# Performance work log

Hardware: AMD Instinct MI355X
Metric: run time of the kernel (lower is better)

## Reference

```python
import jax, jax.numpy as jnp
import numpy as np

LSTM_IN = 125
LSTM_H = 125
MLP_D_H = 512
N = 512


def _lstm_scan(x, Wih, Whh, bih, bhh):
    # x: (N, LSTM_IN); PyTorch gate order: i, f, g, o
    H = LSTM_H
    def step(carry, xt):
        h, c = carry
        g = Wih @ xt + Whh @ h + bih + bhh  # (4H,)
        i = jax.nn.sigmoid(g[:H])
        f = jax.nn.sigmoid(g[H:2 * H])
        gg = jnp.tanh(g[2 * H:3 * H])
        o = jax.nn.sigmoid(g[3 * H:])
        c = f * c + i * gg
        h = o * jnp.tanh(c)
        return (h, c), h
    init = (jnp.zeros((H,), x.dtype), jnp.zeros((H,), x.dtype))
    _, hs = jax.lax.scan(step, init, x)
    return hs  # (N, H)


def setup_inputs() -> dict:
    key = jax.random.key(0)
    ks = jax.random.split(key, 14)
    s = 0.05
    d = {
        "sentence_emb": jax.random.normal(ks[0], (N, 1, LSTM_IN), jnp.float32),
        "Wih_f": jax.random.normal(ks[1], (4 * LSTM_H, LSTM_IN), jnp.float32) * s,
        "Whh_f": jax.random.normal(ks[2], (4 * LSTM_H, LSTM_H), jnp.float32) * s,
        "bih_f": jax.random.normal(ks[3], (4 * LSTM_H,), jnp.float32) * s,
        "bhh_f": jax.random.normal(ks[4], (4 * LSTM_H,), jnp.float32) * s,
        "Wih_b": jax.random.normal(ks[5], (4 * LSTM_H, LSTM_IN), jnp.float32) * s,
        "Whh_b": jax.random.normal(ks[6], (4 * LSTM_H, LSTM_H), jnp.float32) * s,
        "bih_b": jax.random.normal(ks[7], (4 * LSTM_H,), jnp.float32) * s,
        "bhh_b": jax.random.normal(ks[8], (4 * LSTM_H,), jnp.float32) * s,
        "W1": jax.random.normal(ks[9], (MLP_D_H, 4 * LSTM_H), jnp.float32) * s,
        "b1": jax.random.normal(ks[10], (MLP_D_H,), jnp.float32) * s,
        "W2": jax.random.normal(ks[11], (1, MLP_D_H), jnp.float32) * s,
        "b2": jax.random.normal(ks[12], (1,), jnp.float32) * s,
    }
    return d


def reference(sentence_emb, Wih_f, Whh_f, bih_f, bhh_f, Wih_b, Whh_b, bih_b, bhh_b, W1, b1, W2, b2):
    x = sentence_emb[:, 0, :]  # (N, 125), batch=1
    h_fwd = _lstm_scan(x, Wih_f, Whh_f, bih_f, bhh_f)           # (N, 125)
    h_bwd = _lstm_scan(x[::-1], Wih_b, Whh_b, bih_b, bhh_b)[::-1]  # (N, 125)
    h = jnp.concatenate([h_fwd, h_bwd], axis=-1)  # (N, 250)
    # output_mtx[i, j] = MLP(concat(h[j], h[i]))
    # Decompose first linear: W1 @ cat(h_j, h_i) = Wa @ h_j + Wb @ h_i
    D = h.shape[-1]
    Pa = h @ W1[:, :D].T   # (N, H): contribution of h_j
    Pb = h @ W1[:, D:].T   # (N, H): contribution of h_i
    hidden = jnp.tanh(Pb[:, None, :] + Pa[None, :, :] + b1)  # (N, N, H)
    out = hidden @ W2[0] + b2[0]  # (N, N)
    return out
```

## Files before the change

### kernel.cpp

```cpp
#include <hip/hip_runtime.h>

typedef __bf16 bf16_t;
typedef __bf16 bf16x8 __attribute__((ext_vector_type(8)));
typedef float f32x4 __attribute__((ext_vector_type(4)));
typedef int   int4v __attribute__((ext_vector_type(4)));

#define LOG2E 1.4426950408889634f

template<int CTRL>
__device__ __forceinline__ float qperm(float x) {
  return __builtin_bit_cast(float,
      __builtin_amdgcn_update_dpp(0, __builtin_bit_cast(int, x), CTRL, 0xF, 0xF, true));
}

__device__ __forceinline__ void lds_barrier() {
  asm volatile("s_waitcnt lgkmcnt(0)\n\ts_barrier" ::: "memory");
}

__global__ __launch_bounds__(256) void pre_kernel(
    const float* __restrict__ x,
    const float* __restrict__ Wih_f, const float* __restrict__ bih_f,
    const float* __restrict__ bhh_f,
    const float* __restrict__ Wih_b, const float* __restrict__ bih_b,
    const float* __restrict__ bhh_b,
    float* __restrict__ preT)
{
  const int dir = blockIdx.x >> 5;
  const int T   = blockIdx.x & 31;
  const float* __restrict__ Wih = dir ? Wih_b : Wih_f;
  const float* __restrict__ bih = dir ? bih_b : bih_f;
  const float* __restrict__ bhh = dir ? bhh_b : bhh_f;

  const int tid = threadIdx.x;
  const int wv  = tid >> 6;
  const int lane = tid & 63;
  const int q = lane >> 4, cc = lane & 15;

  const int r  = 16 * T + cc;
  const int na = r >> 2, pa = r & 3;
  const bool vld = (na < 125);
  const float* __restrict__ Wr = Wih + (vld ? (125 * pa + na) * 125 : 0);

  bf16x8 whi[4], wlo[4];
  #pragma unroll
  for (int ks = 0; ks < 4; ++ks) {
    #pragma unroll
    for (int j = 0; j < 8; ++j) {
      int k = 32 * ks + 8 * q + j;
      float wvv = (vld && k < 125) ? Wr[k] : 0.0f;
      bf16_t hi = (bf16_t)wvv;
      whi[ks][j] = hi;
      wlo[ks][j] = (bf16_t)(wvv - (float)hi);
    }
  }

  float bias[4];
  #pragma unroll
  for (int reg = 0; reg < 4; ++reg) {
    int ro = 16 * T + 4 * q + reg;
    int no = ro >> 2, po = ro & 3;
    bias[reg] = (no < 125) ? (bih[125 * po + no] + bhh[125 * po + no]) : 0.0f;
  }

  for (int i = 0; i < 8; ++i) {
    const int tt = 8 * wv + i;
    const int t  = 16 * tt + cc;
    const int trow = dir ? (511 - t) : t;
    const float* __restrict__ xr = x + trow * 125;

    f32x4 acc = (f32x4)0.0f;
    #pragma unroll
    for (int ks = 0; ks < 4; ++ks) {
      bf16x8 xhi, xlo;
      #pragma unroll
      for (int j = 0; j < 8; ++j) {
        int k = 32 * ks + 8 * q + j;
        float xv = (k < 125) ? xr[k] : 0.0f;
        bf16_t hi = (bf16_t)xv;
        xhi[j] = hi;
        xlo[j] = (bf16_t)(xv - (float)hi);
      }
      acc = __builtin_amdgcn_mfma_f32_16x16x32_bf16(whi[ks], xhi, acc, 0, 0, 0);
      acc = __builtin_amdgcn_mfma_f32_16x16x32_bf16(whi[ks], xlo, acc, 0, 0, 0);
      acc = __builtin_amdgcn_mfma_f32_16x16x32_bf16(wlo[ks], xhi, acc, 0, 0, 0);
    }
    #pragma unroll
    for (int reg = 0; reg < 4; ++reg) {
      int ro = 16 * T + 4 * q + reg;
      preT[dir * 262144 + ro * 512 + 16 * tt + cc] = acc[reg] + bias[reg];
    }
  }
}

__global__ __launch_bounds__(512) void lstm_kernel(
    const float* __restrict__ Whh_f, const float* __restrict__ Whh_b,
    const float* __restrict__ pre,
    bf16_t* __restrict__ h_all)
{
  const int dir = blockIdx.x;
  const float* __restrict__ Whh = dir ? Whh_b : Whh_f;

  const int tid  = threadIdx.x;
  const int lane = tid & 63;
  const int w    = tid >> 6;
  const int q    = lane >> 4;
  const int cc   = lane & 15;
  const int lt   = cc >> 2;
  const int p    = cc & 3;

  float wm = 0.0f;
  #pragma unroll
  for (int LT = 0; LT < 4; ++LT) {
    int rr = 16 * (4 * w + LT) + cc;
    int nn = rr >> 2, pp = rr & 3;
    if (nn < 125) {
      const float* __restrict__ Wrow = Whh + (125 * pp + nn) * 125;
      #pragma unroll
      for (int ks = 0; ks < 2; ++ks)
        #pragma unroll
        for (int jj = 0; jj < 16; ++jj) {
          int k = 64 * ks + 16 * q + jj;
          if (k < 125) wm = fmaxf(wm, fabsf(Wrow[k]));
        }
    }
  }
  #pragma unroll
  for (int off = 1; off < 64; off <<= 1)
    wm = fmaxf(wm, __shfl_xor(wm, off));
  __shared__ float wmx[8];
  if (lane == 0) wmx[w] = wm;
  __syncthreads();
  float wmax = wmx[0];
  #pragma unroll
  for (int u = 1; u < 8; ++u) wmax = fmaxf(wmax, wmx[u]);
  const float s_w  = 127.0f / wmax;
  const float invq = wmax / (127.0f * 127.0f);

  int4v afrag[4][2];
  #pragma unroll
  for (int LT = 0; LT < 4; ++LT) {
    int rr = 16 * (4 * w + LT) + cc;
    int nn = rr >> 2, pp = rr & 3;
    bool avld = (nn < 125);
    const float* __restrict__ Wrow = Whh + (avld ? (125 * pp + nn) * 125 : 0);
    #pragma unroll
    for (int ks = 0; ks < 2; ++ks) {
      int4v v;
      #pragma unroll
      for (int word = 0; word < 4; ++word) {
        int b = 0;
        #pragma unroll
        for (int byte = 0; byte < 4; ++byte) {
          int jj = 4 * word + byte;
          int k  = 64 * ks + 16 * q + jj;
          int qv = 0;
          if (avld && k < 125)
            qv = (int)__builtin_rintf(Wrow[k] * s_w);
          b |= (qv & 0xFF) << (8 * byte);
        }
        v[word] = b;
      }
      afrag[LT][ks] = v;
    }
  }

  __shared__ __align__(16) char hbuf[2][128];
  if (tid < 256) hbuf[tid >> 7][tid & 127] = 0;
  if (dir == 0) {
    #pragma unroll
    for (int u = 0; u < 6; ++u) h_all[tid * 256 + 250 + u] = (bf16_t)0.0f;
  }
  __syncthreads();

  const int   r_lane = 64 * w + 16 * lt + 4 * q + p;
  const int   nset   = 16 * w + 4 * lt + q;
  const float mult   = (p == 2) ? (-2.0f * LOG2E) : (-LOG2E);
  const float sA     = (p == 2) ? 2.0f : 1.0f;
  const float sB     = (p == 2) ? -1.0f : 0.0f;
  const float dscale = mult * invq;
  const float* __restrict__ preR = pre + dir * 262144 + r_lane * 512;
  float c = 0.0f;

  float4 pv_cur = *(const float4*)preR;

  for (int g = 0; g < 128; ++g) {
    float4 pv_nxt = make_float4(0.f, 0.f, 0.f, 0.f);
    if (g < 127) pv_nxt = *(const float4*)(preR + 4 * (g + 1));

    #pragma unroll
    for (int s4 = 0; s4 < 4; ++s4) {
      const int step = 4 * g + s4;
      const int cur  = s4 & 1, nxt = cur ^ 1;
      const float pv = (s4 == 0) ? pv_cur.x : (s4 == 1) ? pv_cur.y
                     : (s4 == 2) ? pv_cur.z : pv_cur.w;
      const float pvm = mult * pv;

      int4v b0 = *(const int4v*)&hbuf[cur][16 * q];
      int4v b1 = *(const int4v*)&hbuf[cur][64 + 16 * q];

      int4v acc[4];
      #pragma unroll
      for (int LT = 0; LT < 4; ++LT) {
        int4v a = (int4v)0;
        a = __builtin_amdgcn_mfma_i32_16x16x64_i8(afrag[LT][0], b0, a, 0, 0, 0);
        a = __builtin_amdgcn_mfma_i32_16x16x64_i8(afrag[LT][1], b1, a, 0, 0, 0);
        acc[LT] = a;
      }

      int gl[4];
      #pragma unroll
      for (int LT = 0; LT < 4; ++LT) {
        int a01 = (p & 1) ? acc[LT][1] : acc[LT][0];
        int a23 = (p & 1) ? acc[LT][3] : acc[LT][2];
        gl[LT] = (p & 2) ? a23 : a01;
      }
      int b01 = (lt & 1) ? gl[1] : gl[0];
      int b23 = (lt & 1) ? gl[3] : gl[2];
      int gsel = (lt & 2) ? b23 : b01;

      float gf  = (float)gsel;
      float xg  = fmaf(gf, dscale, pvm);
      float e   = __builtin_amdgcn_exp2f(xg);
      float y   = __builtin_amdgcn_rcpf(1.0f + e);
      float act = fmaf(y, sA, sB);

      float b_i = qperm<0x00>(act);
      float b_f = qperm<0x55>(act);
      float b_g = qperm<0xAA>(act);
      float b_o = qperm<0xFF>(act);
      c = fmaf(b_f, c, b_i * b_g);
      float e2 = __builtin_amdgcn_exp2f(-2.0f * LOG2E * c);
      float tc = fmaf(__builtin_amdgcn_rcpf(1.0f + e2), 2.0f, -1.0f);
      float h  = b_o * tc;

      if (p == 0) {
        int qh = (int)__builtin_rintf(h * 127.0f);
        hbuf[nxt][nset] = (char)qh;
        if (nset < 125) {
          int t_orig = dir ? (511 - step) : step;
          h_all[t_orig * 256 + dir * 125 + nset] = (bf16_t)h;
        }
      }
      lds_barrier();
    }
    pv_cur = pv_nxt;
  }
}

__global__ __launch_bounds__(256) void qgemm_kernel(
    const bf16_t* __restrict__ h_all,
    const float* __restrict__ W1,
    const float* __restrict__ b1,
    float* __restrict__ Ea,
    float* __restrict__ Eb)
{
  const int tid  = threadIdx.x;
  const int wv   = tid >> 6;
  const int lane = tid & 63;
  const int q    = lane >> 4, cc = lane & 15;
  const int bj   = blockIdx.x & 31;
  const int bm   = blockIdx.x >> 5;
  const int m    = bm * 64 + wv * 16 + cc;
  const int j0   = bj * 16;
  const int jA   = j0 + cc;

  const bool isB = (m >= 512);
  const int  row = isB ? (m - 512) : m;
  const int  cof = isB ? 250 : 0;

  f32x4 acc = (f32x4)0.0f;
  #pragma unroll
  for (int ks = 0; ks < 8; ++ks) {
    int kb = 32 * ks + 8 * q;
    bf16x8 a = *(const bf16x8*)&h_all[jA * 256 + kb];
    bf16x8 b;
    #pragma unroll
    for (int jj = 0; jj < 8; ++jj) {
      int k = kb + jj;
      float v = (k < 250) ? W1[row * 500 + cof + k] : 0.0f;
      b[jj] = (bf16_t)v;
    }
    acc = __builtin_amdgcn_mfma_f32_16x16x32_bf16(a, b, acc, 0, 0, 0);
  }

  const float C2 = 2.0f * LOG2E;
  #pragma unroll
  for (int reg = 0; reg < 4; ++reg) {
    int j = j0 + 4 * q + reg;
    float v = acc[reg];
    if (!isB) Ea[j * 512 + m] = __builtin_amdgcn_exp2f(C2 * v);
    else      Eb[j * 512 + (m - 512)] =
                  __builtin_amdgcn_exp2f(C2 * (v + b1[m - 512]));
  }
}

__global__ __launch_bounds__(256) void outer_kernel(
    const float* __restrict__ Ea, const float* __restrict__ Eb,
    const float* __restrict__ W2, const float* __restrict__ b2,
    float* __restrict__ out)
{
  __shared__ float sa2[2][32][36];
  __shared__ float sb2[2][16][36];
  __shared__ float sw[2][32];

  const int tid = threadIdx.x;
  const int bi  = blockIdx.x >> 4;
  const int bjx = blockIdx.x & 15;
  const int i0  = bi * 16, j0 = bjx * 32;
  const int ii  = tid & 15;
  const int jj2 = tid >> 4;

  const int lj  = tid & 31, lk4 = (tid >> 5) * 4;
  const int li  = tid & 15, lk4b = ((tid >> 4) & 7) * 4;

  float accR0 = 0.0f, accR1 = 0.0f;
  float wsum = 0.0f;

  for (int kc = 0; kc < 16; ++kc) {
    const int buf = kc & 1;
    const int k0  = kc * 32;
    float4 va = *(const float4*)&Ea[(j0 + lj) * 512 + k0 + lk4];
    *(float4*)&sa2[buf][lj][lk4] = va;
    if (tid < 128) {
      float4 vb = *(const float4*)&Eb[(i0 + li) * 512 + k0 + lk4b];
      *(float4*)&sb2[buf][li][lk4b] = vb;
    }
    if (tid < 32) sw[buf][tid] = W2[k0 + tid];
    __syncthreads();

    #pragma unroll 4
    for (int kk = 0; kk < 32; kk += 2) {
      float2 wv = *(const float2*)&sw[buf][kk];
      float2 bv = *(const float2*)&sb2[buf][ii][kk];
      float2 a0 = *(const float2*)&sa2[buf][2 * jj2 + 0][kk];
      float2 a1 = *(const float2*)&sa2[buf][2 * jj2 + 1][kk];
      wsum += wv.x + wv.y;
      {
        float t1  = fmaf(a0.x, bv.x, 1.0f);
        float t2  = fmaf(a0.y, bv.y, 1.0f);
        float den = t1 * t2;
        float num = fmaf(wv.x, t2, wv.y * t1);
        accR0 = fmaf(num, __builtin_amdgcn_rcpf(den), accR0);
      }
      {
        float t1  = fmaf(a1.x, bv.x, 1.0f);
        float t2  = fmaf(a1.y, bv.y, 1.0f);
        float den = t1 * t2;
        float num = fmaf(wv.x, t2, wv.y * t1);
        accR1 = fmaf(num, __builtin_amdgcn_rcpf(den), accR1);
      }
    }
  }

  const float bb = b2[0];
  float2 o;
  o.x = wsum - 2.0f * accR0 + bb;
  o.y = wsum - 2.0f * accR1 + bb;
  *(float2*)&out[(i0 + ii) * 512 + j0 + 2 * jj2] = o;
}

extern "C" void kernel_launch(void* const* d_in, const int* in_sizes, int n_in,
                              void* d_out, int out_size, void* d_ws, size_t ws_size,
                              hipStream_t stream) {
  const float* emb   = (const float*)d_in[0];
  const float* Wih_f = (const float*)d_in[1];
  const float* Whh_f = (const float*)d_in[2];
  const float* bih_f = (const float*)d_in[3];
  const float* bhh_f = (const float*)d_in[4];
  const float* Wih_b = (const float*)d_in[5];
  const float* Whh_b = (const float*)d_in[6];
  const float* bih_b = (const float*)d_in[7];
  const float* bhh_b = (const float*)d_in[8];
  const float* W1    = (const float*)d_in[9];
  const float* b1    = (const float*)d_in[10];
  const float* W2    = (const float*)d_in[11];
  const float* b2    = (const float*)d_in[12];
  float* out = (float*)d_out;

  char* ws = (char*)d_ws;
  float*  pre   = (float*)ws;
  bf16_t* h_all = (bf16_t*)(ws + 2 * 1024 * 1024);
  float*  Ea    = (float*)(ws + 2 * 1024 * 1024 + 256 * 1024);
  float*  Eb    = Ea + 512 * 512;

  pre_kernel<<<64, 256, 0, stream>>>(emb, Wih_f, bih_f, bhh_f,
                                     Wih_b, bih_b, bhh_b, pre);
  lstm_kernel<<<2, 512, 0, stream>>>(Whh_f, Whh_b, pre, h_all);
  qgemm_kernel<<<512, 256, 0, stream>>>(h_all, W1, b1, Ea, Eb);
  outer_kernel<<<512, 256, 0, stream>>>(Ea, Eb, W2, b2, out);
}
```

Before: 318.9 us.

## Fuse all four stages into one persistent kernel with atomic grid barriers

Merges the input-projection, LSTM recurrence, W1 GEMM and outer MLP kernels into a single 256-block launch separated by software grid barriers built on an atomic counter. The aim is to remove the launch gaps and tail effects between four small kernels, which matter most around the latency-bound LSTM stage. Costs: a memset is added before the launch, the LSTM phase still runs on only two blocks while the rest spin on the barrier, and correctness depends on all 256 blocks of 512 threads being co-resident.

```diff
diff --git a/kernel.cpp b/kernel.cpp
--- a/kernel.cpp
+++ b/kernel.cpp
@@ -6,6 +6,7 @@
 typedef int   int4v __attribute__((ext_vector_type(4)));
 
 #define LOG2E 1.4426950408889634f
+#define NBLK  256
 
 template<int CTRL>
 __device__ __forceinline__ float qperm(float x) {
@@ -17,53 +18,75 @@
   asm volatile("s_waitcnt lgkmcnt(0)\n\ts_barrier" ::: "memory");
 }
 
-__global__ __launch_bounds__(256) void pre_kernel(
+__device__ __forceinline__ void gridbar(unsigned* cnt, unsigned target) {
+  __syncthreads();
+  if (threadIdx.x == 0) {
+    __threadfence();
+    __hip_atomic_fetch_add(cnt, 1u, __ATOMIC_RELEASE, __HIP_MEMORY_SCOPE_AGENT);
+    while (__hip_atomic_load(cnt, __ATOMIC_ACQUIRE, __HIP_MEMORY_SCOPE_AGENT)
+           < target)
+      __builtin_amdgcn_s_sleep(16);
+  }
+  __syncthreads();
+}
+
+__global__ __launch_bounds__(512) void fused_kernel(
     const float* __restrict__ x,
     const float* __restrict__ Wih_f, const float* __restrict__ bih_f,
     const float* __restrict__ bhh_f,
     const float* __restrict__ Wih_b, const float* __restrict__ bih_b,
     const float* __restrict__ bhh_b,
-    float* __restrict__ preT)
+    const float* __restrict__ Whh_f, const float* __restrict__ Whh_b,
+    const float* __restrict__ W1,    const float* __restrict__ b1,
+    const float* __restrict__ W2,    const float* __restrict__ b2,
+    float* __restrict__ preT,
+    bf16_t* __restrict__ h_all,
+    float* __restrict__ Ea,
+    float* __restrict__ Eb,
+    unsigned* __restrict__ cnt,
+    float* __restrict__ out)
 {
-  const int dir = blockIdx.x >> 5;
-  const int T   = blockIdx.x & 31;
-  const float* __restrict__ Wih = dir ? Wih_b : Wih_f;
-  const float* __restrict__ bih = dir ? bih_b : bih_f;
-  const float* __restrict__ bhh = dir ? bhh_b : bhh_f;
-
-  const int tid = threadIdx.x;
-  const int wv  = tid >> 6;
+  const int tid  = threadIdx.x;
+  const int wv   = tid >> 6;
   const int lane = tid & 63;
-  const int q = lane >> 4, cc = lane & 15;
-
-  const int r  = 16 * T + cc;
-  const int na = r >> 2, pa = r & 3;
-  const bool vld = (na < 125);
-  const float* __restrict__ Wr = Wih + (vld ? (125 * pa + na) * 125 : 0);
-
-  bf16x8 whi[4], wlo[4];
-  #pragma unroll
-  for (int ks = 0; ks < 4; ++ks) {
-    #pragma unroll
-    for (int j = 0; j < 8; ++j) {
-      int k = 32 * ks + 8 * q + j;
-      float wvv = (vld && k < 125) ? Wr[k] : 0.0f;
-      bf16_t hi = (bf16_t)wvv;
-      whi[ks][j] = hi;
-      wlo[ks][j] = (bf16_t)(wvv - (float)hi);
-    }
-  }
-
-  float bias[4];
-  #pragma unroll
-  for (int reg = 0; reg < 4; ++reg) {
-    int ro = 16 * T + 4 * q + reg;
-    int no = ro >> 2, po = ro & 3;
-    bias[reg] = (no < 125) ? (bih[125 * po + no] + bhh[125 * po + no]) : 0.0f;
-  }
-
-  for (int i = 0; i < 8; ++i) {
-    const int tt = 8 * wv + i;
+  const int q    = lane >> 4, cc = lane & 15;
+
+  {
+    const int b   = blockIdx.x;
+    const int dir = b >> 7;
+    const int T   = (b >> 2) & 31;
+    const int tq  = b & 3;
+    const float* __restrict__ Wih = dir ? Wih_b : Wih_f;
+    const float* __restrict__ bih = dir ? bih_b : bih_f;
+    const float* __restrict__ bhh = dir ? bhh_b : bhh_f;
+
+    const int r  = 16 * T + cc;
+    const int na = r >> 2, pa = r & 3;
+    const bool vld = (na < 125);
+    const float* __restrict__ Wr = Wih + (vld ? (125 * pa + na) * 125 : 0);
+
+    bf16x8 whi[4], wlo[4];
+    #pragma unroll
+    for (int ks = 0; ks < 4; ++ks) {
+      #pragma unroll
+      for (int j = 0; j < 8; ++j) {
+        int k = 32 * ks + 8 * q + j;
+        float wvv = (vld && k < 125) ? Wr[k] : 0.0f;
+        bf16_t hi = (bf16_t)wvv;
+        whi[ks][j] = hi;
+        wlo[ks][j] = (bf16_t)(wvv - (float)hi);
+      }
+    }
+
+    float bias[4];
+    #pragma unroll
+    for (int reg = 0; reg < 4; ++reg) {
+      int ro = 16 * T + 4 * q + reg;
+      int no = ro >> 2, po = ro & 3;
+      bias[reg] = (no < 125) ? (bih[125 * po + no] + bhh[125 * po + no]) : 0.0f;
+    }
+
+    const int tt = 8 * tq + wv;
     const int t  = 16 * tt + cc;
     const int trow = dir ? (511 - t) : t;
     const float* __restrict__ xr = x + trow * 125;
@@ -90,273 +113,260 @@
       preT[dir * 262144 + ro * 512 + 16 * tt + cc] = acc[reg] + bias[reg];
     }
   }
-}
-
-__global__ __launch_bounds__(512) void lstm_kernel(
-    const float* __restrict__ Whh_f, const float* __restrict__ Whh_b,
-    const float* __restrict__ pre,
-    bf16_t* __restrict__ h_all)
-{
-  const int dir = blockIdx.x;
-  const float* __restrict__ Whh = dir ? Whh_b : Whh_f;
-
-  const int tid  = threadIdx.x;
-  const int lane = tid & 63;
-  const int w    = tid >> 6;
-  const int q    = lane >> 4;
-  const int cc   = lane & 15;
-  const int lt   = cc >> 2;
-  const int p    = cc & 3;
-
-  float wm = 0.0f;
-  #pragma unroll
-  for (int LT = 0; LT < 4; ++LT) {
-    int rr = 16 * (4 * w + LT) + cc;
-    int nn = rr >> 2, pp = rr & 3;
-    if (nn < 125) {
-      const float* __restrict__ Wrow = Whh + (125 * pp + nn) * 125;
-      #pragma unroll
-      for (int ks = 0; ks < 2; ++ks)
+
+  gridbar(cnt, NBLK);
+
+  __shared__ float wmx[8];
+  __shared__ __align__(16) char hbuf[2][128];
+
+  if (blockIdx.x < 2) {
+    const int dir = blockIdx.x;
+    const float* __restrict__ Whh = dir ? Whh_b : Whh_f;
+
+    const int w  = wv;
+    const int lt = cc >> 2;
+    const int p  = cc & 3;
+
+    float wm = 0.0f;
+    #pragma unroll
+    for (int LT = 0; LT < 4; ++LT) {
+      int rr = 16 * (4 * w + LT) + cc;
+      int nn = rr >> 2, pp = rr & 3;
+      if (nn < 125) {
+        const float* __restrict__ Wrow = Whh + (125 * pp + nn) * 125;
         #pragma unroll
-        for (int jj = 0; jj < 16; ++jj) {
-          int k = 64 * ks + 16 * q + jj;
-          if (k < 125) wm = fmaxf(wm, fabsf(Wrow[k]));
-        }
+        for (int ks = 0; ks < 2; ++ks)
+          #pragma unroll
+          for (int jj = 0; jj < 16; ++jj) {
+            int k = 64 * ks + 16 * q + jj;
+            if (k < 125) wm = fmaxf(wm, fabsf(Wrow[k]));
+          }
+      }
+    }
+    #pragma unroll
+    for (int off = 1; off < 64; off <<= 1)
+      wm = fmaxf(wm, __shfl_xor(wm, off));
+    if (lane == 0) wmx[w] = wm;
+    __syncthreads();
+    float wmax = wmx[0];
+    #pragma unroll
+    for (int u = 1; u < 8; ++u) wmax = fmaxf(wmax, wmx[u]);
+    const float s_w  = 127.0f / wmax;
+    const float invq = wmax / (127.0f * 127.0f);
+
+    int4v afrag[4][2];
+    #pragma unroll
+    for (int LT = 0; LT < 4; ++LT) {
+      int rr = 16 * (4 * w + LT) + cc;
+      int nn = rr >> 2, pp = rr & 3;
+      bool avld = (nn < 125);
+      const float* __restrict__ Wrow = Whh + (avld ? (125 * pp + nn) * 125 : 0);
+      #pragma unroll
+      for (int ks = 0; ks < 2; ++ks) {
+        int4v v;
+        #pragma unroll
+        for (int word = 0; word < 4; ++word) {
+          int bb = 0;
+          #pragma unroll
+          for (int byte = 0; byte < 4; ++byte) {
+            int jj = 4 * word + byte;
+            int k  = 64 * ks + 16 * q + jj;
+            int qv = 0;
+            if (avld && k < 125)
+              qv = (int)__builtin_rintf(Wrow[k] * s_w);
+            bb |= (qv & 0xFF) << (8 * byte);
+          }
+          v[word] = bb;
+        }
+        afrag[LT][ks] = v;
+      }
+    }
+
+    if (tid < 256) hbuf[tid >> 7][tid & 127] = 0;
+    if (dir == 0) {
+      #pragma unroll
+      for (int u = 0; u < 6; ++u) h_all[tid * 256 + 250 + u] = (bf16_t)0.0f;
+    }
+    __syncthreads();
+
+    const int   r_lane = 64 * w + 16 * lt + 4 * q + p;
+    const int   nset   = 16 * w + 4 * lt + q;
+    const float mult   = (p == 2) ? (-2.0f * LOG2E) : (-LOG2E);
+    const float sA     = (p == 2) ? 2.0f : 1.0f;
+    const float sB     = (p == 2) ? -1.0f : 0.0f;
+    const float dscale = mult * invq;
+    const float* __restrict__ preR = preT + dir * 262144 + r_lane * 512;
+    float c = 0.0f;
+
+    float4 pv_cur = *(const float4*)preR;
+
+    for (int g = 0; g < 128; ++g) {
+      float4 pv_nxt = make_float4(0.f, 0.f, 0.f, 0.f);
+      if (g < 127) pv_nxt = *(const float4*)(preR + 4 * (g + 1));
+
+      #pragma unroll
+      for (int s4 = 0; s4 < 4; ++s4) {
+        const int step = 4 * g + s4;
+        const int cur  = s4 & 1, nxt = cur ^ 1;
+        const float pv = (s4 == 0) ? pv_cur.x : (s4 == 1) ? pv_cur.y
+                       : (s4 == 2) ? pv_cur.z : pv_cur.w;
+        const float pvm = mult * pv;
+
+        int4v b0 = *(const int4v*)&hbuf[cur][16 * q];
+        int4v b1 = *(const int4v*)&hbuf[cur][64 + 16 * q];
+
+        int4v acc[4];
+        #pragma unroll
+        for (int LT = 0; LT < 4; ++LT) {
+          int4v a = (int4v)0;
+          a = __builtin_amdgcn_mfma_i32_16x16x64_i8(afrag[LT][0], b0, a, 0, 0, 0);
+          a = __builtin_amdgcn_mfma_i32_16x16x64_i8(afrag[LT][1], b1, a, 0, 0, 0);
+          acc[LT] = a;
+        }
+
+        int gl[4];
+        #pragma unroll
+        for (int LT = 0; LT < 4; ++LT) {
+          int a01 = (p & 1) ? acc[LT][1] : acc[LT][0];
+          int a23 = (p & 1) ? acc[LT][3] : acc[LT][2];
+          gl[LT] = (p & 2) ? a23 : a01;
+        }
+        int b01 = (lt & 1) ? gl[1] : gl[0];
+        int b23 = (lt & 1) ? gl[3] : gl[2];
+        int gsel = (lt & 2) ? b23 : b01;
+
+        float gf  = (float)gsel;
+        float xg  = fmaf(gf, dscale, pvm);
+        float e   = __builtin_amdgcn_exp2f(xg);
+        float y   = __builtin_amdgcn_rcpf(1.0f + e);
+        float act = fmaf(y, sA, sB);
+
+        float b_i = qperm<0x00>(act);
+        float b_f = qperm<0x55>(act);
+        float b_g = qperm<0xAA>(act);
+        float b_o = qperm<0xFF>(act);
+        c = fmaf(b_f, c, b_i * b_g);
+        float e2 = __builtin_amdgcn_exp2f(-2.0f * LOG2E * c);
+        float tc = fmaf(__builtin_amdgcn_rcpf(1.0f + e2), 2.0f, -1.0f);
+        float h  = b_o * tc;
+
+        if (p == 0) {
+          int qh = (int)__builtin_rintf(h * 127.0f);
+          hbuf[nxt][nset] = (char)qh;
+          if (nset < 125) {
+            int t_orig = dir ? (511 - step) : step;
+            h_all[t_orig * 256 + dir * 125 + nset] = (bf16_t)h;
+          }
+        }
+        lds_barrier();
+      }
+      pv_cur = pv_nxt;
     }
   }
-  #pragma unroll
-  for (int off = 1; off < 64; off <<= 1)
-    wm = fmaxf(wm, __shfl_xor(wm, off));
-  __shared__ float wmx[8];
-  if (lane == 0) wmx[w] = wm;
-  __syncthreads();
-  float wmax = wmx[0];
-  #pragma unroll
-  for (int u = 1; u < 8; ++u) wmax = fmaxf(wmax, wmx[u]);
-  const float s_w  = 127.0f / wmax;
-  const float invq = wmax / (127.0f * 127.0f);
-
-  int4v afrag[4][2];
-  #pragma unroll
-  for (int LT = 0; LT < 4; ++LT) {
-    int rr = 16 * (4 * w + LT) + cc;
-    int nn = rr >> 2, pp = rr & 3;
-    bool avld = (nn < 125);
-    const float* __restrict__ Wrow = Whh + (avld ? (125 * pp + nn) * 125 : 0);
-    #pragma unroll
-    for (int ks = 0; ks < 2; ++ks) {
-      int4v v;
-      #pragma unroll
-      for (int word = 0; word < 4; ++word) {
-        int b = 0;
-        #pragma unroll
-        for (int byte = 0; byte < 4; ++byte) {
-          int jj = 4 * word + byte;
-          int k  = 64 * ks + 16 * q + jj;
-          int qv = 0;
-          if (avld && k < 125)
-            qv = (int)__builtin_rintf(Wrow[k] * s_w);
-          b |= (qv & 0xFF) << (8 * byte);
-        }
-        v[word] = b;
-      }
-      afrag[LT][ks] = v;
+
+  gridbar(cnt, 2 * NBLK);
+
+  {
+    const int job = blockIdx.x * 8 + wv;
+    const int bj  = job & 31;
+    const int mg  = job >> 5;
+    const int m   = mg * 16 + cc;
+    const int j0  = bj * 16;
+    const int jA  = j0 + cc;
+
+    const bool isB = (m >= 512);
+    const int  row = isB ? (m - 512) : m;
+    const int  cof = isB ? 250 : 0;
+
+    f32x4 acc = (f32x4)0.0f;
+    #pragma unroll
+    for (int ks = 0; ks < 8; ++ks) {
+      int kb = 32 * ks + 8 * q;
+      bf16x8 a = *(const bf16x8*)&h_all[jA * 256 + kb];
+      bf16x8 bfr;
+      #pragma unroll
+      for (int jj = 0; jj < 8; ++jj) {
+        int k = kb + jj;
+        float v = (k < 250) ? W1[row * 500 + cof + k] : 0.0f;
+        bfr[jj] = (bf16_t)v;
+      }
+      acc = __builtin_amdgcn_mfma_f32_16x16x32_bf16(a, bfr, acc, 0, 0, 0);
+    }
+
+    const float C2 = 2.0f * LOG2E;
+    #pragma unroll
+    for (int reg = 0; reg < 4; ++reg) {
+      int j = j0 + 4 * q + reg;
+      float v = acc[reg];
+      if (!isB) Ea[j * 512 + m] = __builtin_amdgcn_exp2f(C2 * v);
+      else      Eb[j * 512 + (m - 512)] =
+                    __builtin_amdgcn_exp2f(C2 * (v + b1[m - 512]));
     }
   }
 
-  __shared__ __align__(16) char hbuf[2][128];
-  if (tid < 256) hbuf[tid >> 7][tid & 127] = 0;
-  if (dir == 0) {
-    #pragma unroll
-    for (int u = 0; u < 6; ++u) h_all[tid * 256 + 250 + u] = (bf16_t)0.0f;
+  gridbar(cnt, 3 * NBLK);
+
+  {
+    __shared__ float sa2[2][2][32][36];
+    __shared__ float sb2[2][2][16][36];
+    __shared__ float sw[2][2][32];
+
+    const int half = tid >> 8;
+    const int t2   = tid & 255;
+    const int job  = blockIdx.x * 2 + half;
+    const int bi   = job >> 4, bjx = job & 15;
+    const int i0   = bi * 16, j0 = bjx * 32;
+    const int ii   = t2 & 15;
+    const int jj2  = t2 >> 4;
+
+    const int lj  = t2 & 31, lk4 = (t2 >> 5) * 4;
+    const int li  = t2 & 15, lk4b = ((t2 >> 4) & 7) * 4;
+
+    float accR0 = 0.0f, accR1 = 0.0f;
+    float wsum = 0.0f;
+
+    for (int kc = 0; kc < 16; ++kc) {
+      const int buf = kc & 1;
+      const int k0  = kc * 32;
+      float4 va = *(const float4*)&Ea[(j0 + lj) * 512 + k0 + lk4];
+      *(float4*)&sa2[half][buf][lj][lk4] = va;
+      if (t2 < 128) {
+        float4 vb = *(const float4*)&Eb[(i0 + li) * 512 + k0 + lk4b];
+        *(float4*)&sb2[half][buf][li][lk4b] = vb;
+      }
+      if (t2 < 32) sw[half][buf][t2] = W2[k0 + t2];
+      __syncthreads();
+
+      #pragma unroll 4
+      for (int kk = 0; kk < 32; kk += 2) {
+        float2 wv2 = *(const float2*)&sw[half][buf][kk];
+        float2 bv  = *(const float2*)&sb2[half][buf][ii][kk];
+        float2 a0  = *(const float2*)&sa2[half][buf][2 * jj2 + 0][kk];
+        float2 a1  = *(const float2*)&sa2[half][buf][2 * jj2 + 1][kk];
+        wsum += wv2.x + wv2.y;
+        {
+          float t1  = fmaf(a0.x, bv.x, 1.0f);
+          float tt2 = fmaf(a0.y, bv.y, 1.0f);
+          float den = t1 * tt2;
+          float num = fmaf(wv2.x, tt2, wv2.y * t1);
+          accR0 = fmaf(num, __builtin_amdgcn_rcpf(den), accR0);
+        }
+        {
+          float t1  = fmaf(a1.x, bv.x, 1.0f);
+          float tt2 = fmaf(a1.y, bv.y, 1.0f);
+          float den = t1 * tt2;
+          float num = fmaf(wv2.x, tt2, wv2.y * t1);
+          accR1 = fmaf(num, __builtin_amdgcn_rcpf(den), accR1);
+        }
+      }
+    }
+
+    const float bb = b2[0];
+    float2 o;
+    o.x = wsum - 2.0f * accR0 + bb;
+    o.y = wsum - 2.0f * accR1 + bb;
+    *(float2*)&out[(i0 + ii) * 512 + j0 + 2 * jj2] = o;
   }
-  __syncthreads();
-
-  const int   r_lane = 64 * w + 16 * lt + 4 * q + p;
-  const int   nset   = 16 * w + 4 * lt + q;
-  const float mult   = (p == 2) ? (-2.0f * LOG2E) : (-LOG2E);
-  const float sA     = (p == 2) ? 2.0f : 1.0f;
-  const float sB     = (p == 2) ? -1.0f : 0.0f;
-  const float dscale = mult * invq;
-  const float* __restrict__ preR = pre + dir * 262144 + r_lane * 512;
-  float c = 0.0f;
-
-  float4 pv_cur = *(const float4*)preR;
-
-  for (int g = 0; g < 128; ++g) {
-    float4 pv_nxt = make_float4(0.f, 0.f, 0.f, 0.f);
-    if (g < 127) pv_nxt = *(const float4*)(preR + 4 * (g + 1));
-
-    #pragma unroll
-    for (int s4 = 0; s4 < 4; ++s4) {
-      const int step = 4 * g + s4;
-      const int cur  = s4 & 1, nxt = cur ^ 1;
-      const float pv = (s4 == 0) ? pv_cur.x : (s4 == 1) ? pv_cur.y
-                     : (s4 == 2) ? pv_cur.z : pv_cur.w;
-      const float pvm = mult * pv;
-
-      int4v b0 = *(const int4v*)&hbuf[cur][16 * q];
-      int4v b1 = *(const int4v*)&hbuf[cur][64 + 16 * q];
-
-      int4v acc[4];
-      #pragma unroll
-      for (int LT = 0; LT < 4; ++LT) {
-        int4v a = (int4v)0;
-        a = __builtin_amdgcn_mfma_i32_16x16x64_i8(afrag[LT][0], b0, a, 0, 0, 0);
-        a = __builtin_amdgcn_mfma_i32_16x16x64_i8(afrag[LT][1], b1, a, 0, 0, 0);
-        acc[LT] = a;
-      }
-
-      int gl[4];
-      #pragma unroll
-      for (int LT = 0; LT < 4; ++LT) {
-        int a01 = (p & 1) ? acc[LT][1] : acc[LT][0];
-        int a23 = (p & 1) ? acc[LT][3] : acc[LT][2];
-        gl[LT] = (p & 2) ? a23 : a01;
-      }
-      int b01 = (lt & 1) ? gl[1] : gl[0];
-      int b23 = (lt & 1) ? gl[3] : gl[2];
-      int gsel = (lt & 2) ? b23 : b01;
-
-      float gf  = (float)gsel;
-      float xg  = fmaf(gf, dscale, pvm);
-      float e   = __builtin_amdgcn_exp2f(xg);
-      float y   = __builtin_amdgcn_rcpf(1.0f + e);
-      float act = fmaf(y, sA, sB);
-
-      float b_i = qperm<0x00>(act);
-      float b_f = qperm<0x55>(act);
-      float b_g = qperm<0xAA>(act);
-      float b_o = qperm<0xFF>(act);
-      c = fmaf(b_f, c, b_i * b_g);
-      float e2 = __builtin_amdgcn_exp2f(-2.0f * LOG2E * c);
-      float tc = fmaf(__builtin_amdgcn_rcpf(1.0f + e2), 2.0f, -1.0f);
-      float h  = b_o * tc;
-
-      if (p == 0) {
-        int qh = (int)__builtin_rintf(h * 127.0f);
-        hbuf[nxt][nset] = (char)qh;
-        if (nset < 125) {
-          int t_orig = dir ? (511 - step) : step;
-          h_all[t_orig * 256 + dir * 125 + nset] = (bf16_t)h;
-        }
-      }
-      lds_barrier();
-    }
-    pv_cur = pv_nxt;
-  }
-}
-
-__global__ __launch_bounds__(256) void qgemm_kernel(
-    const bf16_t* __restrict__ h_all,
-    const float* __restrict__ W1,
-    const float* __restrict__ b1,
-    float* __restrict__ Ea,
-    float* __restrict__ Eb)
-{
-  const int tid  = threadIdx.x;
-  const int wv   = tid >> 6;
-  const int lane = tid & 63;
-  const int q    = lane >> 4, cc = lane & 15;
-  const int bj   = blockIdx.x & 31;
-  const int bm   = blockIdx.x >> 5;
-  const int m    = bm * 64 + wv * 16 + cc;
-  const int j0   = bj * 16;
-  const int jA   = j0 + cc;
-
-  const bool isB = (m >= 512);
-  const int  row = isB ? (m - 512) : m;
-  const int  cof = isB ? 250 : 0;
-
-  f32x4 acc = (f32x4)0.0f;
-  #pragma unroll
-  for (int ks = 0; ks < 8; ++ks) {
-    int kb = 32 * ks + 8 * q;
-    bf16x8 a = *(const bf16x8*)&h_all[jA * 256 + kb];
-    bf16x8 b;
-    #pragma unroll
-    for (int jj = 0; jj < 8; ++jj) {
-      int k = kb + jj;
-      float v = (k < 250) ? W1[row * 500 + cof + k] : 0.0f;
-      b[jj] = (bf16_t)v;
-    }
-    acc = __builtin_amdgcn_mfma_f32_16x16x32_bf16(a, b, acc, 0, 0, 0);
-  }
-
-  const float C2 = 2.0f * LOG2E;
-  #pragma unroll
-  for (int reg = 0; reg < 4; ++reg) {
-    int j = j0 + 4 * q + reg;
-    float v = acc[reg];
-    if (!isB) Ea[j * 512 + m] = __builtin_amdgcn_exp2f(C2 * v);
-    else      Eb[j * 512 + (m - 512)] =
-                  __builtin_amdgcn_exp2f(C2 * (v + b1[m - 512]));
-  }
-}
-
-__global__ __launch_bounds__(256) void outer_kernel(
-    const float* __restrict__ Ea, const float* __restrict__ Eb,
-    const float* __restrict__ W2, const float* __restrict__ b2,
-    float* __restrict__ out)
-{
-  __shared__ float sa2[2][32][36];
-  __shared__ float sb2[2][16][36];
-  __shared__ float sw[2][32];
-
-  const int tid = threadIdx.x;
-  const int bi  = blockIdx.x >> 4;
-  const int bjx = blockIdx.x & 15;
-  const int i0  = bi * 16, j0 = bjx * 32;
-  const int ii  = tid & 15;
-  const int jj2 = tid >> 4;
-
-  const int lj  = tid & 31, lk4 = (tid >> 5) * 4;
-  const int li  = tid & 15, lk4b = ((tid >> 4) & 7) * 4;
-
-  float accR0 = 0.0f, accR1 = 0.0f;
-  float wsum = 0.0f;
-
-  for (int kc = 0; kc < 16; ++kc) {
-    const int buf = kc & 1;
-    const int k0  = kc * 32;
-    float4 va = *(const float4*)&Ea[(j0 + lj) * 512 + k0 + lk4];
-    *(float4*)&sa2[buf][lj][lk4] = va;
-    if (tid < 128) {
-      float4 vb = *(const float4*)&Eb[(i0 + li) * 512 + k0 + lk4b];
-      *(float4*)&sb2[buf][li][lk4b] = vb;
-    }
-    if (tid < 32) sw[buf][tid] = W2[k0 + tid];
-    __syncthreads();
-
-    #pragma unroll 4
-    for (int kk = 0; kk < 32; kk += 2) {
-      float2 wv = *(const float2*)&sw[buf][kk];
-      float2 bv = *(const float2*)&sb2[buf][ii][kk];
-      float2 a0 = *(const float2*)&sa2[buf][2 * jj2 + 0][kk];
-      float2 a1 = *(const float2*)&sa2[buf][2 * jj2 + 1][kk];
-      wsum += wv.x + wv.y;
-      {
-        float t1  = fmaf(a0.x, bv.x, 1.0f);
-        float t2  = fmaf(a0.y, bv.y, 1.0f);
-        float den = t1 * t2;
-        float num = fmaf(wv.x, t2, wv.y * t1);
-        accR0 = fmaf(num, __builtin_amdgcn_rcpf(den), accR0);
-      }
-      {
-        float t1  = fmaf(a1.x, bv.x, 1.0f);
-        float t2  = fmaf(a1.y, bv.y, 1.0f);
-        float den = t1 * t2;
-        float num = fmaf(wv.x, t2, wv.y * t1);
-        accR1 = fmaf(num, __builtin_amdgcn_rcpf(den), accR1);
-      }
-    }
-  }
-
-  const float bb = b2[0];
-  float2 o;
-  o.x = wsum - 2.0f * accR0 + bb;
-  o.y = wsum - 2.0f * accR1 + bb;
-  *(float2*)&out[(i0 + ii) * 512 + j0 + 2 * jj2] = o;
 }
 
 extern "C" void kernel_launch(void* const* d_in, const int* in_sizes, int n_in,
@@ -378,14 +388,15 @@
   float* out = (float*)d_out;
 
   char* ws = (char*)d_ws;
-  float*  pre   = (float*)ws;
-  bf16_t* h_all = (bf16_t*)(ws + 2 * 1024 * 1024);
-  float*  Ea    = (float*)(ws + 2 * 1024 * 1024 + 256 * 1024);
-  float*  Eb    = Ea + 512 * 512;
-
-  pre_kernel<<<64, 256, 0, stream>>>(emb, Wih_f, bih_f, bhh_f,
-                                     Wih_b, bih_b, bhh_b, pre);
-  lstm_kernel<<<2, 512, 0, stream>>>(Whh_f, Whh_b, pre, h_all);
-  qgemm_kernel<<<512, 256, 0, stream>>>(h_all, W1, b1, Ea, Eb);
-  outer_kernel<<<512, 256, 0, stream>>>(Ea, Eb, W2, b2, out);
+  float*    pre   = (float*)ws;
+  bf16_t*   h_all = (bf16_t*)(ws + 2 * 1024 * 1024);
+  float*    Ea    = (float*)(ws + 2 * 1024 * 1024 + 256 * 1024);
+  float*    Eb    = Ea + 512 * 512;
+  unsigned* cnt   = (unsigned*)(ws + 4 * 1024 * 1024 + 256 * 1024 + 160 * 1024);
+
+  hipMemsetAsync(cnt, 0, 64, stream);
+  fused_kernel<<<NBLK, 512, 0, stream>>>(
+      emb, Wih_f, bih_f, bhh_f, Wih_b, bih_b, bhh_b,
+      Whh_f, Whh_b, W1, b1, W2, b2,
+      pre, h_all, Ea, Eb, cnt, out);
 }
```

Result: slower. 1.029 ms (+222.7%).
